# Kernel optimization log

Hardware: AMD Instinct MI355X
Metric: run time of the kernel (lower is better)

Reference implementation:

```python
import jax, jax.numpy as jnp
from jax import lax
import numpy as np

B, C, H, W = 4, 512, 128, 128
K = 19  # n_cls / object regions


def setup_inputs() -> dict:
    key = jax.random.key(0)
    k1, k2, k3 = jax.random.split(key, 3)
    context = jax.random.normal(k1, (B, K, H, W), dtype=jnp.float32)
    feature = jax.random.normal(k2, (B, C, H, W), dtype=jnp.float32)
    w1 = jnp.zeros((C, C, 1, 1), dtype=jnp.float32)  # zero-init per _zero_init_conv
    b1 = jnp.zeros((C,), dtype=jnp.float32)
    w2 = jax.random.normal(k3, (K, 2 * C, 3, 3), dtype=jnp.float32) * 0.02
    b2 = jnp.zeros((K,), dtype=jnp.float32)
    return {"context": context, "feature": feature, "w1": w1, "b1": b1, "w2": w2, "b2": b2}


def reference(context, feature, w1, b1, w2, b2):
    b, c, h, w = feature.shape
    hw = h * w
    f = feature.reshape(b, c, hw).transpose(0, 2, 1)          # [B, HW, C]
    ctx = context.reshape(b, context.shape[1], hw)            # [B, K, HW]
    attn = jax.nn.softmax(ctx, axis=2)                        # softmax over HW
    ocr = jnp.einsum('bkn,bnc->bck', attn, f)                 # ocr_context [B, C, K]
    rel = jnp.einsum('bnc,bck->bkn', f, ocr)                  # relation (already transposed) [B, K, HW]
    attn2 = jax.nn.softmax(rel, axis=2)                       # softmax over HW
    res = jnp.einsum('bck,bkn->bcn', ocr, attn2).reshape(b, c, h, w)
    dn = ('NCHW', 'OIHW', 'NCHW')
    res = lax.conv_general_dilated(res, w1, (1, 1), 'VALID', dimension_numbers=dn)
    res = res + b1[None, :, None, None]
    cat = jnp.concatenate([res, feature], axis=1)             # [B, 2C, H, W]
    out = lax.conv_general_dilated(cat, w2, (1, 1), ((1, 1), (1, 1)), dimension_numbers=dn)
    out = out + b2[None, :, None, None]
    return out
```

## Files before the change

kernel.cpp:

```cpp
#include <hip/hip_runtime.h>
#include <math.h>


typedef _Float16 h2 __attribute__((ext_vector_type(2)));

#define BB 4
#define KK 19
#define CC 512
#define C2 (CC/2)
#define HH 128
#define WW 128
#define HWHW (HH*WW)

__global__ __launch_bounds__(256) void softmax_rows(const float* __restrict__ in,
                                                    float* __restrict__ out) {
    int row = blockIdx.x;
    const float* r = in + (size_t)row * HWHW;
    float* o = out + (size_t)row * HWHW;
    int t = threadIdx.x;
    float v[64];
    float m = -1e30f;
#pragma unroll
    for (int i = 0; i < 64; ++i) { v[i] = r[t + i * 256]; m = fmaxf(m, v[i]); }
    for (int off = 32; off; off >>= 1) m = fmaxf(m, __shfl_xor(m, off));
    __shared__ float sm[4], ss[4];
    int wave = t >> 6;
    if ((t & 63) == 0) sm[wave] = m;
    __syncthreads();
    m = fmaxf(fmaxf(sm[0], sm[1]), fmaxf(sm[2], sm[3]));
    float s = 0.f;
#pragma unroll
    for (int i = 0; i < 64; ++i) { v[i] = __expf(v[i] - m); s += v[i]; }
    for (int off = 32; off; off >>= 1) s += __shfl_xor(s, off);
    if ((t & 63) == 0) ss[wave] = s;
    __syncthreads();
    s = ss[0] + ss[1] + ss[2] + ss[3];
    float inv = 1.f / s;
#pragma unroll
    for (int i = 0; i < 64; ++i) o[t + i * 256] = v[i] * inv;
}

#define NSPLIT 16
__global__ __launch_bounds__(256) void ocr_kernel(const float* __restrict__ feature,
                                                  const float* __restrict__ attn,
                                                  float* __restrict__ ocr,
                                                  h2* __restrict__ fpk) {
    int ctile = blockIdx.x, b = blockIdx.y, ns = blockIdx.z;
    int t = threadIdx.x, wave = t >> 6, lane = t & 63;
    int c0 = ctile * 16 + wave * 4;
    const float* fbase = feature + (size_t)b * CC * HWHW;
    const float* abase = attn + (size_t)b * KK * HWHW;
    h2* fpb = fpk + (size_t)b * C2 * HWHW;
    float acc[4][KK];
#pragma unroll
    for (int j = 0; j < 4; ++j)
#pragma unroll
        for (int k = 0; k < KK; ++k) acc[j][k] = 0.f;
    int nstart = ns * (HWHW / NSPLIT);
    for (int it = 0; it < (HWHW / NSPLIT) / 64; ++it) {
        int n = nstart + it * 64 + lane;
        float a[KK];
#pragma unroll
        for (int k = 0; k < KK; ++k) a[k] = abase[(size_t)k * HWHW + n];
        float fv[4];
#pragma unroll
        for (int j = 0; j < 4; ++j) fv[j] = fbase[(size_t)(c0 + j) * HWHW + n];
        h2 p0, p1;
        p0[0] = (_Float16)fv[0]; p0[1] = (_Float16)fv[1];
        p1[0] = (_Float16)fv[2]; p1[1] = (_Float16)fv[3];
        fpb[(size_t)(c0 >> 1) * HWHW + n] = p0;
        fpb[(size_t)((c0 >> 1) + 1) * HWHW + n] = p1;
#pragma unroll
        for (int j = 0; j < 4; ++j)
#pragma unroll
            for (int k = 0; k < KK; ++k) acc[j][k] += fv[j] * a[k];
    }
#pragma unroll
    for (int j = 0; j < 4; ++j)
#pragma unroll
        for (int k = 0; k < KK; ++k) {
            float x = acc[j][k];
            for (int off = 32; off; off >>= 1) x += __shfl_xor(x, off);
            if (lane == 0) atomicAdd(&ocr[((size_t)b * CC + (c0 + j)) * KK + k], x);
        }
}

__global__ __launch_bounds__(64) void ocr2_kernel(const float* __restrict__ w1,
                                                  const float* __restrict__ ocr,
                                                  float* __restrict__ ocr2) {
    int co = blockIdx.x, b = blockIdx.y, lane = threadIdx.x;
    float acc[KK];
#pragma unroll
    for (int k = 0; k < KK; ++k) acc[k] = 0.f;
    const float* wrow = w1 + (size_t)co * CC;
    const float* ob = ocr + (size_t)b * CC * KK;
    for (int ci = lane; ci < CC; ci += 64) {
        float w = wrow[ci];
#pragma unroll
        for (int k = 0; k < KK; ++k) acc[k] += w * ob[ci * KK + k];
    }
#pragma unroll
    for (int k = 0; k < KK; ++k) {
        float x = acc[k];
        for (int off = 32; off; off >>= 1) x += __shfl_xor(x, off);
        if (lane == 0) ocr2[((size_t)b * CC + co) * KK + k] = x;
    }
}

__global__ __launch_bounds__(256) void wpk_kernel(const float* __restrict__ w2,
                                                  h2* __restrict__ wpk) {
    int idx = blockIdx.x * 256 + threadIdx.x;
    if (idx >= C2 * 171) return;
    int c2 = idx / 171, j = idx % 171;
    int ko = j / 9, tap = j % 9;
    h2 p;
    p[0] = (_Float16)w2[((size_t)ko * (2 * CC) + CC + 2 * c2) * 9 + tap];
    p[1] = (_Float16)w2[((size_t)ko * (2 * CC) + CC + 2 * c2 + 1) * 9 + tap];
    wpk[idx] = p;
}

__global__ __launch_bounds__(256) void opk_kernel(const float* __restrict__ ocr,
                                                  h2* __restrict__ opk) {
    int b = blockIdx.x, c2 = threadIdx.x;
    const float* ob = ocr + (size_t)b * CC * KK;
    h2* op = opk + (size_t)b * C2 * KK;
    for (int k = 0; k < KK; ++k) {
        h2 p;
        p[0] = (_Float16)ob[(2 * c2) * KK + k];
        p[1] = (_Float16)ob[(2 * c2 + 1) * KK + k];
        op[c2 * KK + k] = p;
    }
}

__global__ __launch_bounds__(64) void w2a_kernel(const float* __restrict__ w2,
                                                 const float* __restrict__ ocr2,
                                                 const float* __restrict__ b1,
                                                 float* __restrict__ w2a,
                                                 float* __restrict__ bcon) {
    int ko = blockIdx.x, dydx = blockIdx.y, b = blockIdx.z, lane = threadIdx.x;
    float acc[KK];
#pragma unroll
    for (int k = 0; k < KK; ++k) acc[k] = 0.f;
    float accb = 0.f;
    for (int c = lane; c < CC; c += 64) {
        float wv = w2[((size_t)ko * (2 * CC) + c) * 9 + dydx];
#pragma unroll
        for (int k = 0; k < KK; ++k) acc[k] += wv * ocr2[((size_t)b * CC + c) * KK + k];
        accb += wv * b1[c];
    }
#pragma unroll
    for (int k = 0; k < KK; ++k) {
        float x = acc[k];
        for (int off = 32; off; off >>= 1) x += __shfl_xor(x, off);
        if (lane == 0) w2a[(((size_t)b * KK + ko) * KK + k) * 9 + dydx] = x;
    }
    for (int off = 32; off; off >>= 1) accb += __shfl_xor(accb, off);
    if (lane == 0 && b == 0) bcon[ko * 9 + dydx] = accb;
}

#define NSREL 4
__global__ __launch_bounds__(256) void rel_kernel(const h2* __restrict__ fpk,
                                                  const h2* __restrict__ opk,
                                                  float* __restrict__ rel) {
    int b = blockIdx.y, ns = blockIdx.z;
    int n = blockIdx.x * 256 + threadIdx.x;
    int cb = ns * (C2 / NSREL);
    const h2* fb = fpk + ((size_t)b * C2 + cb) * HWHW + n;
    const h2* ob = opk + ((size_t)b * C2 + cb) * KK;
    float acc[KK];
#pragma unroll
    for (int k = 0; k < KK; ++k) acc[k] = 0.f;
    for (int c2 = 0; c2 < C2 / NSREL; ++c2) {
        h2 f = fb[(size_t)c2 * HWHW];
#pragma unroll
        for (int k = 0; k < KK; ++k)
            acc[k] = __builtin_amdgcn_fdot2(f, ob[c2 * KK + k], acc[k], false);
    }
#pragma unroll
    for (int k = 0; k < KK; ++k)
        atomicAdd(&rel[((size_t)b * KK + k) * HWHW + n], acc[k]);
}

#define NSOUT 8
__global__ __launch_bounds__(256) void out_kernel(const h2* __restrict__ fpk,
                                                  const float* __restrict__ attn2,
                                                  const h2* __restrict__ wpk,
                                                  const float* __restrict__ w2a,
                                                  const float* __restrict__ bcon,
                                                  const float* __restrict__ b2,
                                                  float* __restrict__ out) {
    int b = blockIdx.y, ns = blockIdx.z;
    int t = threadIdx.x;
    int y = blockIdx.x * 2 + (t >> 7);
    int x = t & 127;

    float m[9];
    int off[9];
#pragma unroll
    for (int dy = -1; dy <= 1; ++dy)
#pragma unroll
        for (int dx = -1; dx <= 1; ++dx) {
            int i = (dy + 1) * 3 + (dx + 1);
            int yy = y + dy, xx = x + dx;
            bool valid = (yy >= 0 && yy < HH && xx >= 0 && xx < WW);
            m[i] = valid ? 1.f : 0.f;
            int yc = min(max(yy, 0), HH - 1), xc = min(max(xx, 0), WW - 1);
            off[i] = yc * WW + xc;
        }

    float acc[KK];
#pragma unroll
    for (int ko = 0; ko < KK; ++ko) acc[ko] = 0.f;

    if (ns == 0) {
#pragma unroll
        for (int ko = 0; ko < KK; ++ko) acc[ko] = b2[ko];
#pragma unroll
        for (int i = 0; i < 9; ++i)
#pragma unroll
            for (int ko = 0; ko < KK; ++ko) acc[ko] += m[i] * bcon[ko * 9 + i];
        const float* a2b = attn2 + (size_t)b * KK * HWHW;
        const float* wab = w2a + (size_t)b * KK * KK * 9;
        for (int k = 0; k < KK; ++k) {
            float tap[9];
#pragma unroll
            for (int i = 0; i < 9; ++i) tap[i] = m[i] * a2b[(size_t)k * HWHW + off[i]];
#pragma unroll
            for (int ko = 0; ko < KK; ++ko)
#pragma unroll
                for (int i = 0; i < 9; ++i) acc[ko] += wab[(ko * KK + k) * 9 + i] * tap[i];
        }
    }

    h2 hz; hz[0] = (_Float16)0.f; hz[1] = (_Float16)0.f;
    int cb = ns * (C2 / NSOUT);
    const h2* fb = fpk + ((size_t)b * C2 + cb) * HWHW;
    for (int c2 = 0; c2 < C2 / NSOUT; ++c2) {
        h2 tap2[9];
#pragma unroll
        for (int i = 0; i < 9; ++i)
            tap2[i] = (m[i] != 0.f) ? fb[(size_t)c2 * HWHW + off[i]] : hz;
        const h2* wr = wpk + (cb + c2) * 171;
#pragma unroll
        for (int j = 0; j < 171; ++j)
            acc[j / 9] = __builtin_amdgcn_fdot2(wr[j], tap2[j % 9], acc[j / 9], false);
    }

    size_t obase = ((size_t)b * KK) * HWHW + (size_t)y * WW + x;
#pragma unroll
    for (int ko = 0; ko < KK; ++ko) atomicAdd(&out[obase + (size_t)ko * HWHW], acc[ko]);
}

extern "C" void kernel_launch(void* const* d_in, const int* in_sizes, int n_in,
                              void* d_out, int out_size, void* d_ws, size_t ws_size,
                              hipStream_t stream) {
    const float* ctx = (const float*)d_in[0];
    const float* feature = (const float*)d_in[1];
    const float* w1 = (const float*)d_in[2];
    const float* b1 = (const float*)d_in[3];
    const float* w2 = (const float*)d_in[4];
    const float* b2 = (const float*)d_in[5];
    float* out = (float*)d_out;

    float* ws = (float*)d_ws;
    float* attn = ws;
    float* ocr = attn + (size_t)BB * KK * HWHW;
    float* ocr2 = ocr + (size_t)BB * CC * KK;
    float* w2a = ocr2 + (size_t)BB * CC * KK;
    float* bcon = w2a + (size_t)BB * KK * KK * 9;
    h2* fpk = (h2*)(bcon + KK * 9 + 1);
    h2* opk = fpk + (size_t)BB * C2 * HWHW;
    h2* wpk = opk + (size_t)BB * C2 * KK;

    hipMemsetAsync(ocr, 0, (size_t)BB * CC * KK * sizeof(float), stream);
    hipMemsetAsync(out, 0, (size_t)out_size * sizeof(float), stream);

    softmax_rows<<<BB * KK, 256, 0, stream>>>(ctx, attn);
    ocr_kernel<<<dim3(CC / 16, BB, NSPLIT), 256, 0, stream>>>(feature, attn, ocr, fpk);
    ocr2_kernel<<<dim3(CC, BB), 64, 0, stream>>>(w1, ocr, ocr2);
    wpk_kernel<<<(C2 * 171 + 255) / 256, 256, 0, stream>>>(w2, wpk);
    w2a_kernel<<<dim3(KK, 9, BB), 64, 0, stream>>>(w2, ocr2, b1, w2a, bcon);
    opk_kernel<<<BB, 256, 0, stream>>>(ocr, opk);
    hipMemsetAsync(attn, 0, (size_t)BB * KK * HWHW * sizeof(float), stream);
    rel_kernel<<<dim3(HWHW / 256, BB, NSREL), 256, 0, stream>>>(fpk, opk, attn);
    softmax_rows<<<BB * KK, 256, 0, stream>>>(attn, attn);
    out_kernel<<<dim3(HH / 2, BB, NSOUT), 256, 0, stream>>>(fpk, attn, wpk, w2a, bcon, b2, out);
}
```

Measured before the change: 574.0 us.

## Split attention conv into own kernel, prefetch taps, two pixels per thread in rel

The attn2 part of the 3x3 conv moves out of out_kernel's ns==0 slice into a separate outa_kernel. That kernel writes the output directly, so the output memset goes away and the ns==0 blocks no longer straggle. rel_kernel now handles two pixels per thread with a 4-wide half load and uses twice as many channel splits. Both conv kernels double-buffer their tap loads to overlap memory with compute. The cost is higher register pressure and more atomics in rel.

```diff
diff --git a/kernel.cpp b/kernel.cpp
--- a/kernel.cpp
+++ b/kernel.cpp
@@ -3,6 +3,7 @@
 
 
 typedef _Float16 h2 __attribute__((ext_vector_type(2)));
+typedef _Float16 h4 __attribute__((ext_vector_type(4)));
 
 #define BB 4
 #define KK 19
@@ -158,41 +159,45 @@
     if (lane == 0 && b == 0) bcon[ko * 9 + dydx] = accb;
 }
 
-#define NSREL 4
+#define NSREL 8
 __global__ __launch_bounds__(256) void rel_kernel(const h2* __restrict__ fpk,
                                                   const h2* __restrict__ opk,
                                                   float* __restrict__ rel) {
     int b = blockIdx.y, ns = blockIdx.z;
-    int n = blockIdx.x * 256 + threadIdx.x;
+    int n0 = (blockIdx.x * 256 + threadIdx.x) * 2;
     int cb = ns * (C2 / NSREL);
-    const h2* fb = fpk + ((size_t)b * C2 + cb) * HWHW + n;
+    const h2* fb = fpk + ((size_t)b * C2 + cb) * HWHW;
     const h2* ob = opk + ((size_t)b * C2 + cb) * KK;
-    float acc[KK];
-#pragma unroll
-    for (int k = 0; k < KK; ++k) acc[k] = 0.f;
+    float acc0[KK], acc1[KK];
+#pragma unroll
+    for (int k = 0; k < KK; ++k) { acc0[k] = 0.f; acc1[k] = 0.f; }
+#pragma unroll 4
     for (int c2 = 0; c2 < C2 / NSREL; ++c2) {
-        h2 f = fb[(size_t)c2 * HWHW];
-#pragma unroll
-        for (int k = 0; k < KK; ++k)
-            acc[k] = __builtin_amdgcn_fdot2(f, ob[c2 * KK + k], acc[k], false);
-    }
-#pragma unroll
-    for (int k = 0; k < KK; ++k)
-        atomicAdd(&rel[((size_t)b * KK + k) * HWHW + n], acc[k]);
-}
-
-#define NSOUT 8
-__global__ __launch_bounds__(256) void out_kernel(const h2* __restrict__ fpk,
-                                                  const float* __restrict__ attn2,
-                                                  const h2* __restrict__ wpk,
-                                                  const float* __restrict__ w2a,
-                                                  const float* __restrict__ bcon,
-                                                  const float* __restrict__ b2,
-                                                  float* __restrict__ out) {
-    int b = blockIdx.y, ns = blockIdx.z;
-    int t = threadIdx.x;
-    int y = blockIdx.x * 2 + (t >> 7);
-    int x = t & 127;
+        h4 f = *(const h4*)&fb[(size_t)c2 * HWHW + n0];
+        h2 f0 = __builtin_shufflevector(f, f, 0, 1);
+        h2 f1 = __builtin_shufflevector(f, f, 2, 3);
+#pragma unroll
+        for (int k = 0; k < KK; ++k) {
+            h2 w = ob[c2 * KK + k];
+            acc0[k] = __builtin_amdgcn_fdot2(f0, w, acc0[k], false);
+            acc1[k] = __builtin_amdgcn_fdot2(f1, w, acc1[k], false);
+        }
+    }
+#pragma unroll
+    for (int k = 0; k < KK; ++k) {
+        atomicAdd(&rel[((size_t)b * KK + k) * HWHW + n0], acc0[k]);
+        atomicAdd(&rel[((size_t)b * KK + k) * HWHW + n0 + 1], acc1[k]);
+    }
+}
+
+__global__ __launch_bounds__(256) void outa_kernel(const float* __restrict__ attn2,
+                                                   const float* __restrict__ w2a,
+                                                   const float* __restrict__ bcon,
+                                                   const float* __restrict__ b2,
+                                                   float* __restrict__ out) {
+    int b = blockIdx.y;
+    int px = blockIdx.x * 256 + threadIdx.x;
+    int y = px >> 7, x = px & 127;
 
     float m[9];
     int off[9];
@@ -210,40 +215,83 @@
 
     float acc[KK];
 #pragma unroll
+    for (int ko = 0; ko < KK; ++ko) acc[ko] = b2[ko];
+#pragma unroll
+    for (int i = 0; i < 9; ++i)
+#pragma unroll
+        for (int ko = 0; ko < KK; ++ko) acc[ko] += m[i] * bcon[ko * 9 + i];
+
+    const float* a2b = attn2 + (size_t)b * KK * HWHW;
+    const float* wab = w2a + (size_t)b * KK * KK * 9;
+    float tap[2][9];
+#pragma unroll
+    for (int i = 0; i < 9; ++i) tap[0][i] = m[i] * a2b[off[i]];
+#pragma unroll 2
+    for (int k = 0; k < KK; ++k) {
+        if (k < KK - 1) {
+#pragma unroll
+            for (int i = 0; i < 9; ++i)
+                tap[(k + 1) & 1][i] = m[i] * a2b[(size_t)(k + 1) * HWHW + off[i]];
+        }
+#pragma unroll
+        for (int ko = 0; ko < KK; ++ko)
+#pragma unroll
+            for (int i = 0; i < 9; ++i)
+                acc[ko] += wab[(ko * KK + k) * 9 + i] * tap[k & 1][i];
+    }
+
+    size_t obase = ((size_t)b * KK) * HWHW + (size_t)y * WW + x;
+#pragma unroll
+    for (int ko = 0; ko < KK; ++ko) out[obase + (size_t)ko * HWHW] = acc[ko];
+}
+
+#define NSOUT 8
+__global__ __launch_bounds__(256) void out_kernel(const h2* __restrict__ fpk,
+                                                  const h2* __restrict__ wpk,
+                                                  float* __restrict__ out) {
+    int b = blockIdx.y, ns = blockIdx.z;
+    int t = threadIdx.x;
+    int y = blockIdx.x * 2 + (t >> 7);
+    int x = t & 127;
+
+    float m[9];
+    int off[9];
+#pragma unroll
+    for (int dy = -1; dy <= 1; ++dy)
+#pragma unroll
+        for (int dx = -1; dx <= 1; ++dx) {
+            int i = (dy + 1) * 3 + (dx + 1);
+            int yy = y + dy, xx = x + dx;
+            bool valid = (yy >= 0 && yy < HH && xx >= 0 && xx < WW);
+            m[i] = valid ? 1.f : 0.f;
+            int yc = min(max(yy, 0), HH - 1), xc = min(max(xx, 0), WW - 1);
+            off[i] = yc * WW + xc;
+        }
+
+    float acc[KK];
+#pragma unroll
     for (int ko = 0; ko < KK; ++ko) acc[ko] = 0.f;
-
-    if (ns == 0) {
-#pragma unroll
-        for (int ko = 0; ko < KK; ++ko) acc[ko] = b2[ko];
-#pragma unroll
-        for (int i = 0; i < 9; ++i)
-#pragma unroll
-            for (int ko = 0; ko < KK; ++ko) acc[ko] += m[i] * bcon[ko * 9 + i];
-        const float* a2b = attn2 + (size_t)b * KK * HWHW;
-        const float* wab = w2a + (size_t)b * KK * KK * 9;
-        for (int k = 0; k < KK; ++k) {
-            float tap[9];
-#pragma unroll
-            for (int i = 0; i < 9; ++i) tap[i] = m[i] * a2b[(size_t)k * HWHW + off[i]];
-#pragma unroll
-            for (int ko = 0; ko < KK; ++ko)
-#pragma unroll
-                for (int i = 0; i < 9; ++i) acc[ko] += wab[(ko * KK + k) * 9 + i] * tap[i];
-        }
-    }
 
     h2 hz; hz[0] = (_Float16)0.f; hz[1] = (_Float16)0.f;
     int cb = ns * (C2 / NSOUT);
     const h2* fb = fpk + ((size_t)b * C2 + cb) * HWHW;
+
+    h2 tap[2][9];
+#pragma unroll
+    for (int i = 0; i < 9; ++i)
+        tap[0][i] = (m[i] != 0.f) ? fb[off[i]] : hz;
+#pragma unroll 2
     for (int c2 = 0; c2 < C2 / NSOUT; ++c2) {
-        h2 tap2[9];
-#pragma unroll
-        for (int i = 0; i < 9; ++i)
-            tap2[i] = (m[i] != 0.f) ? fb[(size_t)c2 * HWHW + off[i]] : hz;
-        const h2* wr = wpk + (cb + c2) * 171;
+        if (c2 < C2 / NSOUT - 1) {
+#pragma unroll
+            for (int i = 0; i < 9; ++i)
+                tap[(c2 + 1) & 1][i] =
+                    (m[i] != 0.f) ? fb[(size_t)(c2 + 1) * HWHW + off[i]] : hz;
+        }
+        const h2* wr = wpk + (size_t)(cb + c2) * 171;
 #pragma unroll
         for (int j = 0; j < 171; ++j)
-            acc[j / 9] = __builtin_amdgcn_fdot2(wr[j], tap2[j % 9], acc[j / 9], false);
+            acc[j / 9] = __builtin_amdgcn_fdot2(wr[j], tap[c2 & 1][j % 9], acc[j / 9], false);
     }
 
     size_t obase = ((size_t)b * KK) * HWHW + (size_t)y * WW + x;
@@ -273,7 +321,6 @@
     h2* wpk = opk + (size_t)BB * C2 * KK;
 
     hipMemsetAsync(ocr, 0, (size_t)BB * CC * KK * sizeof(float), stream);
-    hipMemsetAsync(out, 0, (size_t)out_size * sizeof(float), stream);
 
     softmax_rows<<<BB * KK, 256, 0, stream>>>(ctx, attn);
     ocr_kernel<<<dim3(CC / 16, BB, NSPLIT), 256, 0, stream>>>(feature, attn, ocr, fpk);
@@ -282,7 +329,8 @@
     w2a_kernel<<<dim3(KK, 9, BB), 64, 0, stream>>>(w2, ocr2, b1, w2a, bcon);
     opk_kernel<<<BB, 256, 0, stream>>>(ocr, opk);
     hipMemsetAsync(attn, 0, (size_t)BB * KK * HWHW * sizeof(float), stream);
-    rel_kernel<<<dim3(HWHW / 256, BB, NSREL), 256, 0, stream>>>(fpk, opk, attn);
+    rel_kernel<<<dim3(HWHW / 512, BB, NSREL), 256, 0, stream>>>(fpk, opk, attn);
     softmax_rows<<<BB * KK, 256, 0, stream>>>(attn, attn);
-    out_kernel<<<dim3(HH / 2, BB, NSOUT), 256, 0, stream>>>(fpk, attn, wpk, w2a, bcon, b2, out);
-}
+    outa_kernel<<<dim3(HWHW / 256, BB), 256, 0, stream>>>(attn, w2a, bcon, b2, out);
+    out_kernel<<<dim3(HH / 2, BB, NSOUT), 256, 0, stream>>>(fpk, wpk, out);
+}
```

Measured after the change: 706.1 us. +23.0%, slower.

## Split output conv into attention-part kernel and LDS-tiled feature conv

Applied to the files above, without the earlier changes.

Moves the attention-derived 3x3 conv term (bias, bcon, attn2 x w2a) into a separate outa_kernel. That kernel writes the output directly, so the output memset is no longer needed, and it software-pipelines the tap loads across k. The feature 3x3 conv now stages 4 rows of packed fp16 feature tiles in shared memory with zero halos, and reads the 9 taps from LDS instead of issuing 9 global loads per channel pair. This removes the load imbalance where the ns==0 blocks did the extra attention work, at the cost of an extra launch and syncthreads per sub-chunk.

```diff
diff --git a/kernel.cpp b/kernel.cpp
--- a/kernel.cpp
+++ b/kernel.cpp
@@ -181,18 +181,14 @@
         atomicAdd(&rel[((size_t)b * KK + k) * HWHW + n], acc[k]);
 }
 
-#define NSOUT 8
-__global__ __launch_bounds__(256) void out_kernel(const h2* __restrict__ fpk,
-                                                  const float* __restrict__ attn2,
-                                                  const h2* __restrict__ wpk,
-                                                  const float* __restrict__ w2a,
-                                                  const float* __restrict__ bcon,
-                                                  const float* __restrict__ b2,
-                                                  float* __restrict__ out) {
-    int b = blockIdx.y, ns = blockIdx.z;
-    int t = threadIdx.x;
-    int y = blockIdx.x * 2 + (t >> 7);
-    int x = t & 127;
+__global__ __launch_bounds__(256) void outa_kernel(const float* __restrict__ attn2,
+                                                   const float* __restrict__ w2a,
+                                                   const float* __restrict__ bcon,
+                                                   const float* __restrict__ b2,
+                                                   float* __restrict__ out) {
+    int b = blockIdx.y;
+    int px = blockIdx.x * 256 + threadIdx.x;
+    int y = px >> 7, x = px & 127;
 
     float m[9];
     int off[9];
@@ -210,43 +206,94 @@
 
     float acc[KK];
 #pragma unroll
+    for (int ko = 0; ko < KK; ++ko) acc[ko] = b2[ko];
+#pragma unroll
+    for (int i = 0; i < 9; ++i)
+#pragma unroll
+        for (int ko = 0; ko < KK; ++ko) acc[ko] += m[i] * bcon[ko * 9 + i];
+
+    const float* a2b = attn2 + (size_t)b * KK * HWHW;
+    const float* wab = w2a + (size_t)b * KK * KK * 9;
+    float tap[2][9];
+#pragma unroll
+    for (int i = 0; i < 9; ++i) tap[0][i] = m[i] * a2b[off[i]];
+#pragma unroll 2
+    for (int k = 0; k < KK; ++k) {
+        if (k < KK - 1) {
+#pragma unroll
+            for (int i = 0; i < 9; ++i)
+                tap[(k + 1) & 1][i] = m[i] * a2b[(size_t)(k + 1) * HWHW + off[i]];
+        }
+#pragma unroll
+        for (int ko = 0; ko < KK; ++ko)
+#pragma unroll
+            for (int i = 0; i < 9; ++i)
+                acc[ko] += wab[(ko * KK + k) * 9 + i] * tap[k & 1][i];
+    }
+
+    size_t obase = ((size_t)b * KK) * HWHW + (size_t)y * WW + x;
+#pragma unroll
+    for (int ko = 0; ko < KK; ++ko) out[obase + (size_t)ko * HWHW] = acc[ko];
+}
+
+#define NSOUT 8
+#define SUBC 8
+__global__ __launch_bounds__(256) void out_kernel(const h2* __restrict__ fpk,
+                                                  const h2* __restrict__ wpk,
+                                                  float* __restrict__ out) {
+    __shared__ h2 st[SUBC * 4 * 130];
+    int b = blockIdx.y, ns = blockIdx.z;
+    int t = threadIdx.x;
+    int w = t >> 7;
+    int x = t & 127;
+    int y0 = blockIdx.x * 2;
+
+    h2 hz; hz[0] = (_Float16)0.f; hz[1] = (_Float16)0.f;
+
+    if (t < SUBC * 4 * 2) {
+        int c2r = t >> 1;
+        int side = t & 1;
+        st[c2r * 130 + side * 129] = hz;
+    }
+
+    int cb = ns * (C2 / NSOUT);
+    const h2* fbase = fpk + ((size_t)b * C2 + cb) * HWHW;
+
+    float acc[KK];
+#pragma unroll
     for (int ko = 0; ko < KK; ++ko) acc[ko] = 0.f;
 
-    if (ns == 0) {
-#pragma unroll
-        for (int ko = 0; ko < KK; ++ko) acc[ko] = b2[ko];
-#pragma unroll
-        for (int i = 0; i < 9; ++i)
-#pragma unroll
-            for (int ko = 0; ko < KK; ++ko) acc[ko] += m[i] * bcon[ko * 9 + i];
-        const float* a2b = attn2 + (size_t)b * KK * HWHW;
-        const float* wab = w2a + (size_t)b * KK * KK * 9;
-        for (int k = 0; k < KK; ++k) {
-            float tap[9];
-#pragma unroll
-            for (int i = 0; i < 9; ++i) tap[i] = m[i] * a2b[(size_t)k * HWHW + off[i]];
-#pragma unroll
-            for (int ko = 0; ko < KK; ++ko)
-#pragma unroll
-                for (int i = 0; i < 9; ++i) acc[ko] += wab[(ko * KK + k) * 9 + i] * tap[i];
-        }
-    }
-
-    h2 hz; hz[0] = (_Float16)0.f; hz[1] = (_Float16)0.f;
-    int cb = ns * (C2 / NSOUT);
-    const h2* fb = fpk + ((size_t)b * C2 + cb) * HWHW;
-    for (int c2 = 0; c2 < C2 / NSOUT; ++c2) {
-        h2 tap2[9];
-#pragma unroll
-        for (int i = 0; i < 9; ++i)
-            tap2[i] = (m[i] != 0.f) ? fb[(size_t)c2 * HWHW + off[i]] : hz;
-        const h2* wr = wpk + (cb + c2) * 171;
-#pragma unroll
-        for (int j = 0; j < 171; ++j)
-            acc[j / 9] = __builtin_amdgcn_fdot2(wr[j], tap2[j % 9], acc[j / 9], false);
-    }
-
-    size_t obase = ((size_t)b * KK) * HWHW + (size_t)y * WW + x;
+    for (int ch = 0; ch < (C2 / NSOUT) / SUBC; ++ch) {
+        __syncthreads();
+#pragma unroll
+        for (int e = 0; e < (SUBC * 4 * 128) / 256; ++e) {
+            int idx = e * 256 + t;
+            int c2s = idx >> 9;
+            int rem = idx & 511;
+            int r = rem >> 7;
+            int xx = rem & 127;
+            int yy = y0 - 1 + r;
+            h2 v = hz;
+            if (yy >= 0 && yy < HH)
+                v = fbase[(size_t)(ch * SUBC + c2s) * HWHW + yy * WW + xx];
+            st[(c2s * 4 + r) * 130 + xx + 1] = v;
+        }
+        __syncthreads();
+        for (int c2s = 0; c2s < SUBC; ++c2s) {
+            h2 tp[9];
+#pragma unroll
+            for (int dy = 0; dy < 3; ++dy)
+#pragma unroll
+                for (int dx = 0; dx < 3; ++dx)
+                    tp[dy * 3 + dx] = st[(c2s * 4 + w + dy) * 130 + x + dx];
+            const h2* wr = wpk + (size_t)(cb + ch * SUBC + c2s) * 171;
+#pragma unroll
+            for (int j = 0; j < 171; ++j)
+                acc[j / 9] = __builtin_amdgcn_fdot2(wr[j], tp[j % 9], acc[j / 9], false);
+        }
+    }
+
+    size_t obase = ((size_t)b * KK) * HWHW + (size_t)(y0 + w) * WW + x;
 #pragma unroll
     for (int ko = 0; ko < KK; ++ko) atomicAdd(&out[obase + (size_t)ko * HWHW], acc[ko]);
 }
@@ -273,7 +320,6 @@
     h2* wpk = opk + (size_t)BB * C2 * KK;
 
     hipMemsetAsync(ocr, 0, (size_t)BB * CC * KK * sizeof(float), stream);
-    hipMemsetAsync(out, 0, (size_t)out_size * sizeof(float), stream);
 
     softmax_rows<<<BB * KK, 256, 0, stream>>>(ctx, attn);
     ocr_kernel<<<dim3(CC / 16, BB, NSPLIT), 256, 0, stream>>>(feature, attn, ocr, fpk);
@@ -284,5 +330,6 @@
     hipMemsetAsync(attn, 0, (size_t)BB * KK * HWHW * sizeof(float), stream);
     rel_kernel<<<dim3(HWHW / 256, BB, NSREL), 256, 0, stream>>>(fpk, opk, attn);
     softmax_rows<<<BB * KK, 256, 0, stream>>>(attn, attn);
-    out_kernel<<<dim3(HH / 2, BB, NSOUT), 256, 0, stream>>>(fpk, attn, wpk, w2a, bcon, b2, out);
-}
+    outa_kernel<<<dim3(HWHW / 256, BB), 256, 0, stream>>>(attn, w2a, bcon, b2, out);
+    out_kernel<<<dim3(HH / 2, BB, NSOUT), 256, 0, stream>>>(fpk, wpk, out);
+}
```

After: 565.8 us. Within noise of the previous version (-1.4%).
